# Performance work log

Hardware: AMD Instinct MI355X
Metric: run time of the kernel (lower is better)

The kernel has to match this reference:

```python
import jax, jax.numpy as jnp
import numpy as np

N, E, F, DE, G, C = 50000, 800000, 64, 32, 512, 2
EPS = 1e-5


def setup_inputs() -> dict:
    key = jax.random.key(0)
    ks = jax.random.split(key, 12)
    Z = 2 * F + DE  # CGConv concat dim [x_i, x_j, edge_attr]
    inp = {
        "x": jax.random.normal(ks[0], (N, F), dtype=jnp.float32),
        "edge_index": jax.random.randint(ks[1], (2, E), 0, N, dtype=jnp.int32),
        "edge_attr": jax.random.normal(ks[2], (E, DE), dtype=jnp.float32),
        "batch": jnp.sort(jax.random.randint(ks[3], (N,), 0, G, dtype=jnp.int32)),
        # CGConv lin_f / lin_s : (2F+De) -> F, with bias
        "Wf": jax.random.normal(ks[4], (Z, F), dtype=jnp.float32) * 0.05,
        "bf": jnp.zeros((F,), dtype=jnp.float32),
        "Ws": jax.random.normal(ks[5], (Z, F), dtype=jnp.float32) * 0.05,
        "bs": jnp.zeros((F,), dtype=jnp.float32),
        # CGConv internal BatchNorm (training-mode batch stats)
        "bn_w": jnp.ones((F,), dtype=jnp.float32),
        "bn_b": jnp.zeros((F,), dtype=jnp.float32),
        # PyG LayerNorm (graph mode, batch=None -> whole-tensor stats)
        "ln_w": jnp.ones((F,), dtype=jnp.float32),
        "ln_b": jnp.zeros((F,), dtype=jnp.float32),
        # final linear (2F -> C) and output LayerNorm
        "Wl": jax.random.normal(ks[6], (2 * F, C), dtype=jnp.float32) * 0.05,
        "bl": jnp.zeros((C,), dtype=jnp.float32),
        "ln4_w": jnp.ones((C,), dtype=jnp.float32),
        "ln4_b": jnp.zeros((C,), dtype=jnp.float32),
    }
    return inp


def _pyg_layernorm(x, w, b):
    # torch_geometric.nn.LayerNorm, mode='graph', batch=None: whole-tensor stats
    xc = x - jnp.mean(x)
    out = xc / (jnp.sqrt(jnp.mean(xc * xc)) + EPS)
    return out * w + b


def reference(x, edge_index, edge_attr, batch, Wf, bf, Ws, bs, bn_w, bn_b,
              ln_w, ln_b, Wl, bl, ln4_w, ln4_b):
    src = edge_index[0]  # x_j (source)
    dst = edge_index[1]  # x_i (target / aggregation index)

    # CGConv message: sigmoid(lin_f(z)) * softplus(lin_s(z)), z=[x_i,x_j,e]
    z = jnp.concatenate([x[dst], x[src], edge_attr], axis=1)  # [E, 2F+De]
    msg = jax.nn.sigmoid(z @ Wf + bf) * jax.nn.softplus(z @ Ws + bs)  # [E,F]

    # scatter-add aggregation to target nodes
    agg = jax.ops.segment_sum(msg, dst, num_segments=N)  # [N,F]

    # CGConv batch_norm=True (training-mode batch statistics over nodes)
    mu = jnp.mean(agg, axis=0)
    var = jnp.mean((agg - mu) ** 2, axis=0)
    agg = (agg - mu) / jnp.sqrt(var + EPS) * bn_w + bn_b

    # residual
    h = agg + x

    # LayerNorm + softplus
    h = jax.nn.softplus(_pyg_layernorm(h, ln_w, ln_b))

    # global mean / add pooling over graphs
    add_pool = jax.ops.segment_sum(h, batch, num_segments=G)  # [G,F]
    counts = jax.ops.segment_sum(jnp.ones((N,), h.dtype), batch, num_segments=G)
    mean_pool = add_pool / jnp.maximum(counts, 1.0)[:, None]

    g = jnp.concatenate([mean_pool, add_pool], axis=1)  # [G, 2F]
    out = g @ Wl + bl  # [G, C]
    out = _pyg_layernorm(out, ln4_w, ln4_b)
    return out
```

## Files before the change

kernel.cpp:

```cpp
#include <hip/hip_runtime.h>
#include <math.h>

#define EPSF 1e-5f

typedef short bf16x8 __attribute__((ext_vector_type(8)));
typedef float f32x4 __attribute__((ext_vector_type(4)));

static __device__ __forceinline__ unsigned short f2bf(float x) {
  unsigned u = __float_as_uint(x);
  unsigned r = (u + 0x7FFFu + ((u >> 16) & 1u)) >> 16;
  return (unsigned short)r;
}

static __device__ __forceinline__ float msgv(float F, float S) {
  float sig = __builtin_amdgcn_rcpf(1.0f + __expf(-F));
  float sp = fmaxf(S, 0.f) + __logf(1.0f + __expf(-fabsf(S)));
  return sig * sp;
}

static __device__ __forceinline__ void gload16(const void* g, void* l) {
  __builtin_amdgcn_global_load_lds(
      (const __attribute__((address_space(1))) unsigned int*)g,
      (__attribute__((address_space(3))) unsigned int*)l, 16, 0, 0);
}

__global__ __launch_bounds__(256) void prep_kernel(
    const float* __restrict__ x, const float* __restrict__ Wf,
    const float* __restrict__ Ws, const int* __restrict__ ei,
    unsigned short* __restrict__ xbf, unsigned short* __restrict__ Bfrag,
    int* __restrict__ deg, int NCV, int total8, int E) {
  const int b = blockIdx.x, t = threadIdx.x;
  if (b < NCV) {
    int i = b * 256 + t;
    if (i < total8) {
      float4 a = ((const float4*)x)[i * 2];
      float4 c = ((const float4*)x)[i * 2 + 1];
      unsigned short o[8];
      o[0] = f2bf(a.x); o[1] = f2bf(a.y); o[2] = f2bf(a.z); o[3] = f2bf(a.w);
      o[4] = f2bf(c.x); o[5] = f2bf(c.y); o[6] = f2bf(c.z); o[7] = f2bf(c.w);
      ((uint4*)xbf)[i] = *(uint4*)o;
    }
  } else if (b < NCV + 10) {
    int g2 = (b - NCV) * 256 + t;
    if (g2 < 2560) {
      const int ks = g2 >> 9, t8 = (g2 >> 6) & 7, l = g2 & 63;
      const int q = l & 15, g = l >> 4;
      const float* W = (t8 < 4) ? Wf : Ws;
      const int col = (t8 & 3) * 16 + q;
      unsigned short out[8];
#pragma unroll
      for (int i = 0; i < 8; ++i) {
        int kk = ks * 32 + g * 8 + i;
        int wr = (kk < 32) ? (128 + kk) : (kk - 32);
        out[i] = f2bf(W[(size_t)wr * 64 + col]);
      }
      *(uint4*)&Bfrag[((size_t)(ks * 8 + t8) * 64 + l) * 8] = *(uint4*)out;
    }
  } else {
    int i = (b - NCV - 10) * 256 + t;
    if (i < E) atomicAdd(&deg[ei[E + i]], 1);
  }
}

__global__ __launch_bounds__(256) void scan_a(const int* __restrict__ deg,
                                              int* __restrict__ bsum, int N) {
  const int idx = blockIdx.x * 256 + threadIdx.x;
  int v = (idx < N) ? ((deg[idx] + 15) >> 4) : 0;
#pragma unroll
  for (int o = 32; o > 0; o >>= 1) v += __shfl_down(v, o);
  __shared__ int ws4[4];
  if ((threadIdx.x & 63) == 0) ws4[threadIdx.x >> 6] = v;
  __syncthreads();
  if (threadIdx.x == 0) bsum[blockIdx.x] = ws4[0] + ws4[1] + ws4[2] + ws4[3];
}

__global__ __launch_bounds__(256) void scan_b(const int* __restrict__ bsum,
                                              int* __restrict__ bpre,
                                              int* __restrict__ tile_total,
                                              int NB) {
  const int t = threadIdx.x;
  const int lane = t & 63, w = t >> 6;
  int v = (t < NB) ? bsum[t] : 0;
  int sc = v;
#pragma unroll
  for (int o = 1; o < 64; o <<= 1) {
    int u = __shfl_up(sc, o);
    if (lane >= o) sc += u;
  }
  __shared__ int wsum[4];
  if (lane == 63) wsum[w] = sc;
  __syncthreads();
  int add = 0;
#pragma unroll
  for (int k = 0; k < 4; ++k) add += (k < w) ? wsum[k] : 0;
  bpre[t] = (sc - v) + add;
  if (t == 255) tile_total[0] = sc + add;
}

__global__ __launch_bounds__(256) void scan_c(const int* __restrict__ deg,
                                              const int* __restrict__ bpre,
                                              int* __restrict__ cursor,
                                              int* __restrict__ tstart, int N) {
  const int t = threadIdx.x;
  const int lane = t & 63, w = t >> 6;
  const int idx = blockIdx.x * 256 + t;
  int d = (idx < N) ? ((deg[idx] + 15) >> 4) : 0;
  int sc = d;
#pragma unroll
  for (int o = 1; o < 64; o <<= 1) {
    int u = __shfl_up(sc, o);
    if (lane >= o) sc += u;
  }
  __shared__ int wsum[4];
  if (lane == 63) wsum[w] = sc;
  __syncthreads();
  int add = bpre[blockIdx.x];
#pragma unroll
  for (int k = 0; k < 4; ++k) add += (k < w) ? wsum[k] : 0;
  if (idx < N) {
    int ts = add + (sc - d);
    tstart[idx] = ts;
    cursor[idx] = ts * 16;
  }
}

__global__ __launch_bounds__(256) void scatter_pack(
    const int* __restrict__ ei, int* __restrict__ cursor,
    const int* __restrict__ deg, const int* __restrict__ tstart,
    const float* __restrict__ eattr, int* __restrict__ epk,
    int* __restrict__ thdr, unsigned short* __restrict__ eabf, int E) {
  int i = blockIdx.x * 256 + threadIdx.x;
  if (i >= E) return;
  const int src = ei[i];
  const int dst = ei[E + i];
  const int pos = atomicAdd(&cursor[dst], 1);
  epk[pos] = (src & 0xFFFF) | (dst << 16);
  const int ts = tstart[dst];
  const int k = pos - ts * 16;
  if ((k & 15) == 0) {
    int vc = min(16, deg[dst] - (k & ~15));
    thdr[ts + (k >> 4)] = dst | (vc << 16);
  }
  const float4* er = (const float4*)(eattr + (size_t)i * 32);
  unsigned short o[32];
#pragma unroll
  for (int kk = 0; kk < 8; ++kk) {
    float4 v = er[kk];
    o[kk * 4] = f2bf(v.x); o[kk * 4 + 1] = f2bf(v.y);
    o[kk * 4 + 2] = f2bf(v.z); o[kk * 4 + 3] = f2bf(v.w);
  }
  uint4* dp = (uint4*)(eabf + (size_t)pos * 32);
#pragma unroll
  for (int kk = 0; kk < 4; ++kk) dp[kk] = ((uint4*)o)[kk];
}

__global__ __launch_bounds__(256) void edge_fused(
    const int* __restrict__ epk, const int* __restrict__ thdr,
    const unsigned short* __restrict__ eabf,
    const unsigned short* __restrict__ xbf,
    const unsigned short* __restrict__ Bfrag, const float* __restrict__ bf_,
    const float* __restrict__ bs_, float* __restrict__ agg,
    const int* __restrict__ tile_total, int N) {
  __shared__ __align__(16) unsigned char Bls[40960];
  __shared__ __align__(16) unsigned char AshA[40960];

  for (int i = threadIdx.x; i < 2560; i += 256)
    ((uint4*)Bls)[i] = ((const uint4*)Bfrag)[i];
  __syncthreads();

  const int lane = threadIdx.x & 63, w = threadIdx.x >> 6;
  const int q = lane & 15, g = lane >> 4;
  const int row = lane >> 2, c = lane & 3;
  const int cs = c ^ ((row >> 1) & 3);

  const int T = tile_total[0];
  const int nB = gridDim.x;
  const int cb = (blockIdx.x & 7) * (nB >> 3) + (blockIdx.x >> 3);
  const int qT = T / nB, rT = T - qT * nB;
  const int bt0 = cb * qT + min(cb, rT);
  const int bt1 = bt0 + qT + (cb < rT ? 1 : 0);
  const int blen = bt1 - bt0;
  const int per = (blen + 3) >> 2;
  const int wt0 = bt0 + w * per;
  const int wt1 = min(bt1, wt0 + per);
  if (wt0 >= wt1) return;
  const int tlast = wt1 - 1;

  float bfv[4], bsv[4];
#pragma unroll
  for (int cg = 0; cg < 4; ++cg) {
    bfv[cg] = bf_[cg * 16 + q];
    bsv[cg] = bs_[cg * 16 + q];
  }

  char* myA = (char*)AshA + w * 10240;

  auto STAGE = [&](int bufSel, int tile, int er) {
    unsigned su = (unsigned)(er & 0xFFFF);
    if (su >= (unsigned)N) su = 0;
    unsigned du = ((unsigned)er) >> 16;
    if (du >= (unsigned)N) du = 0;
    char* base = myA + bufSel * 5120;
    gload16(eabf + ((size_t)tile * 16 + row) * 32 + cs * 8, base);
    gload16(xbf + (size_t)du * 64 + cs * 8, base + 1024);
    gload16(xbf + (size_t)du * 64 + 32 + cs * 8, base + 2048);
    gload16(xbf + (size_t)su * 64 + cs * 8, base + 3072);
    gload16(xbf + (size_t)su * 64 + 32 + cs * 8, base + 4096);
  };

  atomicAdd(&agg[lane], 0.0f);
  int tcur = wt0;
  int ep_c = epk[(size_t)tcur * 16 + row];
  int hdr_cur = thdr[tcur];
  STAGE(0, tcur, ep_c);
  const int t1i = min(tcur + 1, tlast);
  int ep_next = epk[(size_t)t1i * 16 + row];
  int hdr_next = thdr[t1i];
  int buf = 0;

  for (;;) {
    const int tn = min(tcur + 1, tlast);
    const int t2i = min(tcur + 2, tlast);
    STAGE(buf ^ 1, tn, ep_next);
    int ep_nn = epk[(size_t)t2i * 16 + row];
    int hdr_nn = thdr[t2i];
    __builtin_amdgcn_sched_barrier(0);
    asm volatile("s_waitcnt vmcnt(8)" ::: "memory");
    __builtin_amdgcn_sched_barrier(0);

    const char* Ab = myA + buf * 5120;
    f32x4 accf[4], accs[4];
#pragma unroll
    for (int nt = 0; nt < 4; ++nt) {
      accf[nt] = (f32x4){0.f, 0.f, 0.f, 0.f};
      accs[nt] = (f32x4){0.f, 0.f, 0.f, 0.f};
    }
#pragma unroll
    for (int ks = 0; ks < 5; ++ks) {
      const bf16x8 a =
          *(const bf16x8*)(Ab + ks * 1024 + q * 64 + ((g ^ ((q >> 1) & 3)) << 4));
#pragma unroll
      for (int nt = 0; nt < 4; ++nt) {
        const bf16x8 Bfr =
            *(const bf16x8*)(Bls + (((ks * 8 + nt) * 64 + lane) << 4));
        const bf16x8 Bsr =
            *(const bf16x8*)(Bls + (((ks * 8 + 4 + nt) * 64 + lane) << 4));
        accf[nt] =
            __builtin_amdgcn_mfma_f32_16x16x32_bf16(a, Bfr, accf[nt], 0, 0, 0);
        accs[nt] =
            __builtin_amdgcn_mfma_f32_16x16x32_bf16(a, Bsr, accs[nt], 0, 0, 0);
      }
    }

    const int dstT = hdr_cur & 0xFFFF;
    const int vcnt = hdr_cur >> 16;
    float tot0, tot1, tot2, tot3;
#pragma unroll
    for (int cg = 0; cg < 4; ++cg) {
      float s = 0.f;
#pragma unroll
      for (int r = 0; r < 4; ++r) {
        float m = msgv(accf[cg][r] + bfv[cg], accs[cg][r] + bsv[cg]);
        s += (g * 4 + r < vcnt) ? m : 0.f;
      }
      s += __shfl_xor(s, 16);
      s += __shfl_xor(s, 32);
      if (cg == 0) tot0 = s;
      else if (cg == 1) tot1 = s;
      else if (cg == 2) tot2 = s;
      else tot3 = s;
    }
    float v = (g == 0) ? tot0 : (g == 1) ? tot1 : (g == 2) ? tot2 : tot3;
    unsigned dd = (unsigned)dstT;
    float vv = (dd < (unsigned)N) ? v : 0.f;
    dd = min(dd, (unsigned)(N - 1));
    atomicAdd(&agg[(size_t)dd * 64 + g * 16 + q], vv);

    if (tcur == tlast) break;
    tcur += 1;
    buf ^= 1;
    hdr_cur = hdr_next;
    hdr_next = hdr_nn;
    ep_next = ep_nn;
  }
}

__global__ __launch_bounds__(256) void stats_kernel(
    const float* __restrict__ agg, const float* __restrict__ x,
    float* __restrict__ stats, int N) {
  const int f = threadIdx.x & 63;
  const int sub = threadIdx.x >> 6;
  float sa = 0, sa2 = 0, sx = 0, sx2 = 0, sax = 0;
  for (int r = blockIdx.x * 4 + sub; r < N; r += gridDim.x * 4) {
    float a = agg[(size_t)r * 64 + f];
    float xv = x[(size_t)r * 64 + f];
    sa += a; sa2 += a * a; sx += xv; sx2 += xv * xv; sax += a * xv;
  }
  __shared__ float lds[4][5][64];
  lds[sub][0][f] = sa; lds[sub][1][f] = sa2; lds[sub][2][f] = sx;
  lds[sub][3][f] = sx2; lds[sub][4][f] = sax;
  __syncthreads();
  if (sub == 0) {
#pragma unroll
    for (int i = 0; i < 5; ++i) {
      float v = lds[0][i][f] + lds[1][i][f] + lds[2][i][f] + lds[3][i][f];
      atomicAdd(&stats[i * 64 + f], v);
    }
  }
}

__global__ __launch_bounds__(256) void node_finish(
    const float* __restrict__ stats, const float* __restrict__ bn_w,
    const float* __restrict__ bn_b, const float* __restrict__ agg,
    const float* __restrict__ x, const int* __restrict__ batch,
    const float* __restrict__ ln_w, const float* __restrict__ ln_b,
    float* __restrict__ add_pool, float* __restrict__ counts, int N,
    int chunk) {
  const int f = threadIdx.x & 63;
  const int sub = threadIdx.x >> 6;
  const float Nf = (float)N;
  const float invN = 1.0f / Nf;
  float Sa = stats[f], Sa2 = stats[64 + f], Sx = stats[128 + f],
        Sx2 = stats[192 + f], Sax = stats[256 + f];
  float mu = Sa * invN;
  float var = Sa2 * invN - mu * mu;
  const float alpha = bn_w[f] / sqrtf(var + EPSF);
  const float beta = bn_b[f] - mu * alpha;
  float Sh = alpha * Sa + Nf * beta + Sx;
  float Sh2 = alpha * alpha * Sa2 + Sx2 + Nf * beta * beta +
              2.f * alpha * Sax + 2.f * alpha * beta * Sa + 2.f * beta * Sx;
#pragma unroll
  for (int o = 32; o > 0; o >>= 1) {
    Sh += __shfl_xor(Sh, o);
    Sh2 += __shfl_xor(Sh2, o);
  }
  const float cnt = Nf * 64.0f;
  const float mean = Sh / cnt;
  const float msq = Sh2 / cnt - mean * mean;
  const float rden = 1.0f / (sqrtf(fmaxf(msq, 0.f)) + EPSF);
  const float lw = ln_w[f] * rden;
  const float lb = ln_b[f];

  const int r0 = blockIdx.x * chunk;
  const int r1 = min(N, r0 + chunk);
  float acc = 0.f, cacc = 0.f;
  int curg = -1;
  for (int r = r0 + sub; r < r1; r += 4) {
    int g = batch[r];
    if (g != curg) {
      if (curg >= 0) {
        atomicAdd(&add_pool[(size_t)curg * 64 + f], acc);
        if (f == 0) atomicAdd(&counts[curg], cacc);
      }
      curg = g; acc = 0.f; cacc = 0.f;
    }
    float h = fmaf(alpha, agg[(size_t)r * 64 + f], beta) + x[(size_t)r * 64 + f];
    float v = (h - mean) * lw + lb;
    float sp = fmaxf(v, 0.f) + __logf(1.0f + __expf(-fabsf(v)));
    acc += sp; cacc += 1.f;
  }
  if (curg >= 0) {
    atomicAdd(&add_pool[(size_t)curg * 64 + f], acc);
    if (f == 0) atomicAdd(&counts[curg], cacc);
  }
}

__global__ __launch_bounds__(1024) void graph_out(
    const float* __restrict__ add_pool, const float* __restrict__ counts,
    const float* __restrict__ Wl, const float* __restrict__ bl,
    const float* __restrict__ w4, const float* __restrict__ b4,
    float* __restrict__ out, int G) {
  const int t = threadIdx.x;
  const int g = t >> 1, c = t & 1;
  float cnt = fmaxf(counts[g], 1.0f);
  float inv = 1.0f / cnt;
  const float4* ap4 = (const float4*)(add_pool + (size_t)g * 64);
  const float4* W4 = (const float4*)Wl;
  float v = bl[c];
#pragma unroll 4
  for (int k4 = 0; k4 < 16; ++k4) {
    float4 a4 = ap4[k4];
    float4 wa = W4[k4 * 2];
    float4 wb = W4[k4 * 2 + 1];
    float4 wc = W4[32 + k4 * 2];
    float4 wd = W4[32 + k4 * 2 + 1];
    float m0 = c ? wa.y : wa.x, m1 = c ? wa.w : wa.z;
    float m2 = c ? wb.y : wb.x, m3 = c ? wb.w : wb.z;
    float a0 = c ? wc.y : wc.x, a1 = c ? wc.w : wc.z;
    float a2 = c ? wd.y : wd.x, a3 = c ? wd.w : wd.z;
    v = fmaf(a4.x, fmaf(m0, inv, a0), v);
    v = fmaf(a4.y, fmaf(m1, inv, a1), v);
    v = fmaf(a4.z, fmaf(m2, inv, a2), v);
    v = fmaf(a4.w, fmaf(m3, inv, a3), v);
  }

  __shared__ float red[16];
  __shared__ float bc[2];
  float sum = v;
#pragma unroll
  for (int o = 32; o > 0; o >>= 1) sum += __shfl_down(sum, o);
  if ((t & 63) == 0) red[t >> 6] = sum;
  __syncthreads();
  if (t == 0) {
    float tot = 0;
#pragma unroll
    for (int i = 0; i < 16; ++i) tot += red[i];
    bc[0] = tot * (1.0f / 1024.0f);
  }
  __syncthreads();
  const float mean = bc[0];
  const float xc = v - mean;
  float sq = xc * xc;
  __syncthreads();
#pragma unroll
  for (int o = 32; o > 0; o >>= 1) sq += __shfl_down(sq, o);
  if ((t & 63) == 0) red[t >> 6] = sq;
  __syncthreads();
  if (t == 0) {
    float tot = 0;
#pragma unroll
    for (int i = 0; i < 16; ++i) tot += red[i];
    bc[1] = 1.0f / (sqrtf(tot * (1.0f / 1024.0f)) + EPSF);
  }
  __syncthreads();
  out[t] = xc * bc[1] * w4[c] + b4[c];
}

extern "C" void kernel_launch(void* const* d_in, const int* in_sizes, int n_in,
                              void* d_out, int out_size, void* d_ws,
                              size_t ws_size, hipStream_t stream) {
  const float* x = (const float*)d_in[0];
  const int* ei = (const int*)d_in[1];
  const float* eattr = (const float*)d_in[2];
  const int* batch = (const int*)d_in[3];
  const float* Wf = (const float*)d_in[4];
  const float* bf = (const float*)d_in[5];
  const float* Ws = (const float*)d_in[6];
  const float* bs = (const float*)d_in[7];
  const float* bn_w = (const float*)d_in[8];
  const float* bn_b = (const float*)d_in[9];
  const float* ln_w = (const float*)d_in[10];
  const float* ln_b = (const float*)d_in[11];
  const float* Wl = (const float*)d_in[12];
  const float* bl = (const float*)d_in[13];
  const float* w4 = (const float*)d_in[14];
  const float* b4 = (const float*)d_in[15];

  const int N = in_sizes[0] / 64;
  const int E = in_sizes[2] / 32;
  const int G = 512;
  const int NB = (N + 255) / 256;
  const int NCV = (N * 8 + 255) / 256;
  const int NH = (E + 255) / 256;
  const int Tcap = N + (E + 15) / 16;

  float* ws = (float*)d_ws;
  float* agg = ws;
  float* stats = agg + (size_t)N * 64;
  float* add_pool = stats + 320;
  float* counts = add_pool + (size_t)G * 64;
  int* deg = (int*)(counts + G);
  int* cursor = deg + N;
  int* tstart = cursor + N;
  int* tile_total = tstart + N;
  int* bsum = tile_total + 4;
  int* bpre = bsum + 256;
  unsigned short* Bfrag = (unsigned short*)(bpre + 256);
  unsigned short* xbf = Bfrag + 20480;
  int* thdr = (int*)(xbf + (size_t)N * 64);
  int* epk = thdr + Tcap;
  unsigned short* eabf = (unsigned short*)(epk + (size_t)Tcap * 16);

  size_t zeroFloats = (size_t)N * 64 + 320 + (size_t)G * 64 + G + N;
  hipMemsetAsync(agg, 0, zeroFloats * sizeof(float), stream);
  hipMemsetAsync(epk, 0, (size_t)Tcap * 16 * sizeof(int), stream);

  prep_kernel<<<NCV + 10 + NH, 256, 0, stream>>>(x, Wf, Ws, ei, xbf, Bfrag,
                                                 deg, NCV, N * 8, E);
  scan_a<<<NB, 256, 0, stream>>>(deg, bsum, N);
  scan_b<<<1, 256, 0, stream>>>(bsum, bpre, tile_total, NB);
  scan_c<<<NB, 256, 0, stream>>>(deg, bpre, cursor, tstart, N);
  scatter_pack<<<NH, 256, 0, stream>>>(ei, cursor, deg, tstart, eattr, epk,
                                       thdr, eabf, E);
  edge_fused<<<512, 256, 0, stream>>>(epk, thdr, eabf, xbf, Bfrag, bf, bs, agg,
                                      tile_total, N);
  stats_kernel<<<512, 256, 0, stream>>>(agg, x, stats, N);
  const int chunk = (N + 511) / 512;
  node_finish<<<512, 256, 0, stream>>>(stats, bn_w, bn_b, agg, x, batch, ln_w,
                                       ln_b, add_pool, counts, N, chunk);
  graph_out<<<1, 1024, 0, stream>>>(add_pool, counts, Wl, bl, w4, b4,
                                    (float*)d_out, G);
}
```

Measured before the change: 323.1 us.

## Precompute per-node destination projection and drop x_i from the edge GEMM

Every edge in a tile shares the same destination node, so the x_i part of lin_f and lin_s (plus bias) is computed once per node by a new node_mfma kernel into a float2 buffer. The edge kernel then runs a 96-wide K GEMM (edge_attr plus x_j) instead of 160, stages less data into LDS, and adds the per-node projection loaded from global memory. LDS use per block drops, so the edge grid is raised from 512 to 768 blocks. The cost is an extra kernel launch and a 25.6MB float2 buffer, now written once and read per tile, and the vmcnt wait is retuned to match the new load count.

```diff
diff --git a/kernel.cpp b/kernel.cpp
--- a/kernel.cpp
+++ b/kernel.cpp
@@ -28,7 +28,8 @@
     const float* __restrict__ x, const float* __restrict__ Wf,
     const float* __restrict__ Ws, const int* __restrict__ ei,
     unsigned short* __restrict__ xbf, unsigned short* __restrict__ Bfrag,
-    int* __restrict__ deg, int NCV, int total8, int E) {
+    unsigned short* __restrict__ Bfrag2, int* __restrict__ deg, int NCV,
+    int total8, int E) {
   const int b = blockIdx.x, t = threadIdx.x;
   if (b < NCV) {
     int i = b * 256 + t;
@@ -40,9 +41,9 @@
       o[4] = f2bf(c.x); o[5] = f2bf(c.y); o[6] = f2bf(c.z); o[7] = f2bf(c.w);
       ((uint4*)xbf)[i] = *(uint4*)o;
     }
-  } else if (b < NCV + 10) {
+  } else if (b < NCV + 6) {
     int g2 = (b - NCV) * 256 + t;
-    if (g2 < 2560) {
+    if (g2 < 1536) {
       const int ks = g2 >> 9, t8 = (g2 >> 6) & 7, l = g2 & 63;
       const int q = l & 15, g = l >> 4;
       const float* W = (t8 < 4) ? Wf : Ws;
@@ -51,14 +52,71 @@
 #pragma unroll
       for (int i = 0; i < 8; ++i) {
         int kk = ks * 32 + g * 8 + i;
-        int wr = (kk < 32) ? (128 + kk) : (kk - 32);
+        int wr = (kk < 32) ? (128 + kk) : (32 + kk);
         out[i] = f2bf(W[(size_t)wr * 64 + col]);
       }
       *(uint4*)&Bfrag[((size_t)(ks * 8 + t8) * 64 + l) * 8] = *(uint4*)out;
     }
+  } else if (b < NCV + 10) {
+    int g2 = (b - NCV - 6) * 256 + t;
+    if (g2 < 1024) {
+      const int ks = g2 >> 9, t8 = (g2 >> 6) & 7, l = g2 & 63;
+      const int q = l & 15, g = l >> 4;
+      const float* W = (t8 < 4) ? Wf : Ws;
+      const int col = (t8 & 3) * 16 + q;
+      unsigned short out[8];
+#pragma unroll
+      for (int i = 0; i < 8; ++i) {
+        int kk = ks * 32 + g * 8 + i;
+        out[i] = f2bf(W[(size_t)kk * 64 + col]);
+      }
+      *(uint4*)&Bfrag2[((size_t)(ks * 8 + t8) * 64 + l) * 8] = *(uint4*)out;
+    }
   } else {
     int i = (b - NCV - 10) * 256 + t;
     if (i < E) atomicAdd(&deg[ei[E + i]], 1);
+  }
+}
+
+__global__ __launch_bounds__(256, 4) void node_mfma(
+    const unsigned short* __restrict__ xbf,
+    const unsigned short* __restrict__ Bfrag2, const float* __restrict__ bf_,
+    const float* __restrict__ bs_, float2* __restrict__ Pd2, int N) {
+  __shared__ __align__(16) short Bsh[16][64][8];
+  for (int i = threadIdx.x; i < 1024; i += 256)
+    ((uint4*)Bsh)[i] = ((const uint4*)Bfrag2)[i];
+  __syncthreads();
+  const int lane = threadIdx.x & 63, w = threadIdx.x >> 6;
+  const int q = lane & 15, g = lane >> 4;
+  const int row0 = blockIdx.x * 64;
+  const float bfv = bf_[w * 16 + q], bsv = bs_[w * 16 + q];
+  f32x4 accf[4], accs[4];
+#pragma unroll
+  for (int mt = 0; mt < 4; ++mt) {
+    accf[mt] = (f32x4){0.f, 0.f, 0.f, 0.f};
+    accs[mt] = (f32x4){0.f, 0.f, 0.f, 0.f};
+  }
+#pragma unroll
+  for (int ks = 0; ks < 2; ++ks) {
+    const bf16x8 Bfr = *(const bf16x8*)&Bsh[ks * 8 + w][lane][0];
+    const bf16x8 Bsr = *(const bf16x8*)&Bsh[ks * 8 + 4 + w][lane][0];
+#pragma unroll
+    for (int mt = 0; mt < 4; ++mt) {
+      int row = min(row0 + mt * 16 + q, N - 1);
+      const bf16x8 a = *(const bf16x8*)(xbf + (size_t)row * 64 + ks * 32 + g * 8);
+      accf[mt] = __builtin_amdgcn_mfma_f32_16x16x32_bf16(a, Bfr, accf[mt], 0, 0, 0);
+      accs[mt] = __builtin_amdgcn_mfma_f32_16x16x32_bf16(a, Bsr, accs[mt], 0, 0, 0);
+    }
+  }
+#pragma unroll
+  for (int mt = 0; mt < 4; ++mt) {
+#pragma unroll
+    for (int r = 0; r < 4; ++r) {
+      int row = row0 + mt * 16 + g * 4 + r;
+      if (row < N)
+        Pd2[(size_t)row * 64 + w * 16 + q] =
+            make_float2(accf[mt][r] + bfv, accs[mt][r] + bsv);
+    }
   }
 }
 
@@ -158,13 +216,12 @@
     const int* __restrict__ epk, const int* __restrict__ thdr,
     const unsigned short* __restrict__ eabf,
     const unsigned short* __restrict__ xbf,
-    const unsigned short* __restrict__ Bfrag, const float* __restrict__ bf_,
-    const float* __restrict__ bs_, float* __restrict__ agg,
-    const int* __restrict__ tile_total, int N) {
-  __shared__ __align__(16) unsigned char Bls[40960];
-  __shared__ __align__(16) unsigned char AshA[40960];
-
-  for (int i = threadIdx.x; i < 2560; i += 256)
+    const unsigned short* __restrict__ Bfrag, const float2* __restrict__ Pd2,
+    float* __restrict__ agg, const int* __restrict__ tile_total, int N) {
+  __shared__ __align__(16) unsigned char Bls[24576];
+  __shared__ __align__(16) unsigned char AshA[24576];
+
+  for (int i = threadIdx.x; i < 1536; i += 256)
     ((uint4*)Bls)[i] = ((const uint4*)Bfrag)[i];
   __syncthreads();
 
@@ -186,49 +243,43 @@
   if (wt0 >= wt1) return;
   const int tlast = wt1 - 1;
 
-  float bfv[4], bsv[4];
-#pragma unroll
-  for (int cg = 0; cg < 4; ++cg) {
-    bfv[cg] = bf_[cg * 16 + q];
-    bsv[cg] = bs_[cg * 16 + q];
-  }
-
-  char* myA = (char*)AshA + w * 10240;
-
-  auto STAGE = [&](int bufSel, int tile, int er) {
+  char* myA = (char*)AshA + w * 6144;
+
+  auto STAGE = [&](int bufSel, int tile, int er, int hdr, float2 (&pd)[4]) {
     unsigned su = (unsigned)(er & 0xFFFF);
     if (su >= (unsigned)N) su = 0;
-    unsigned du = ((unsigned)er) >> 16;
+    unsigned du = (unsigned)(hdr & 0xFFFF);
     if (du >= (unsigned)N) du = 0;
-    char* base = myA + bufSel * 5120;
+    char* base = myA + bufSel * 3072;
     gload16(eabf + ((size_t)tile * 16 + row) * 32 + cs * 8, base);
-    gload16(xbf + (size_t)du * 64 + cs * 8, base + 1024);
-    gload16(xbf + (size_t)du * 64 + 32 + cs * 8, base + 2048);
-    gload16(xbf + (size_t)su * 64 + cs * 8, base + 3072);
-    gload16(xbf + (size_t)su * 64 + 32 + cs * 8, base + 4096);
+    gload16(xbf + (size_t)su * 64 + cs * 8, base + 1024);
+    gload16(xbf + (size_t)su * 64 + 32 + cs * 8, base + 2048);
+#pragma unroll
+    for (int nt = 0; nt < 4; ++nt) pd[nt] = Pd2[(size_t)du * 64 + nt * 16 + q];
   };
 
   atomicAdd(&agg[lane], 0.0f);
   int tcur = wt0;
+  int hdr_cur = thdr[tcur];
   int ep_c = epk[(size_t)tcur * 16 + row];
-  int hdr_cur = thdr[tcur];
-  STAGE(0, tcur, ep_c);
+  float2 pd_cur[4], pd_nxt[4];
+  STAGE(0, tcur, ep_c, hdr_cur, pd_cur);
   const int t1i = min(tcur + 1, tlast);
-  int ep_next = epk[(size_t)t1i * 16 + row];
-  int hdr_next = thdr[t1i];
+  int ep_n = epk[(size_t)t1i * 16 + row];
+  int hdr_n = thdr[t1i];
   int buf = 0;
 
   for (;;) {
     const int tn = min(tcur + 1, tlast);
     const int t2i = min(tcur + 2, tlast);
-    STAGE(buf ^ 1, tn, ep_next);
+    STAGE(buf ^ 1, tn, ep_n, hdr_n, pd_nxt);
     int ep_nn = epk[(size_t)t2i * 16 + row];
     int hdr_nn = thdr[t2i];
     __builtin_amdgcn_sched_barrier(0);
-    asm volatile("s_waitcnt vmcnt(8)" ::: "memory");
+    asm volatile("s_waitcnt vmcnt(15)" ::: "memory");
     __builtin_amdgcn_sched_barrier(0);
 
-    const char* Ab = myA + buf * 5120;
+    const char* Ab = myA + buf * 3072;
     f32x4 accf[4], accs[4];
 #pragma unroll
     for (int nt = 0; nt < 4; ++nt) {
@@ -236,7 +287,7 @@
       accs[nt] = (f32x4){0.f, 0.f, 0.f, 0.f};
     }
 #pragma unroll
-    for (int ks = 0; ks < 5; ++ks) {
+    for (int ks = 0; ks < 3; ++ks) {
       const bf16x8 a =
           *(const bf16x8*)(Ab + ks * 1024 + q * 64 + ((g ^ ((q >> 1) & 3)) << 4));
 #pragma unroll
@@ -260,7 +311,7 @@
       float s = 0.f;
 #pragma unroll
       for (int r = 0; r < 4; ++r) {
-        float m = msgv(accf[cg][r] + bfv[cg], accs[cg][r] + bsv[cg]);
+        float m = msgv(accf[cg][r] + pd_cur[cg].x, accs[cg][r] + pd_cur[cg].y);
         s += (g * 4 + r < vcnt) ? m : 0.f;
       }
       s += __shfl_xor(s, 16);
@@ -279,9 +330,11 @@
     if (tcur == tlast) break;
     tcur += 1;
     buf ^= 1;
-    hdr_cur = hdr_next;
-    hdr_next = hdr_nn;
-    ep_next = ep_nn;
+    hdr_cur = hdr_n;
+    hdr_n = hdr_nn;
+    ep_n = ep_nn;
+#pragma unroll
+    for (int nt = 0; nt < 4; ++nt) pd_cur[nt] = pd_nxt[nt];
   }
 }
 
@@ -466,8 +519,10 @@
   int* bsum = tile_total + 4;
   int* bpre = bsum + 256;
   unsigned short* Bfrag = (unsigned short*)(bpre + 256);
-  unsigned short* xbf = Bfrag + 20480;
-  int* thdr = (int*)(xbf + (size_t)N * 64);
+  unsigned short* Bfrag2 = Bfrag + 12288;
+  unsigned short* xbf = Bfrag2 + 8192;
+  float2* Pd2 = (float2*)(xbf + (size_t)N * 64);
+  int* thdr = (int*)(Pd2 + (size_t)N * 64);
   int* epk = thdr + Tcap;
   unsigned short* eabf = (unsigned short*)(epk + (size_t)Tcap * 16);
 
@@ -476,13 +531,14 @@
   hipMemsetAsync(epk, 0, (size_t)Tcap * 16 * sizeof(int), stream);
 
   prep_kernel<<<NCV + 10 + NH, 256, 0, stream>>>(x, Wf, Ws, ei, xbf, Bfrag,
-                                                 deg, NCV, N * 8, E);
+                                                 Bfrag2, deg, NCV, N * 8, E);
+  node_mfma<<<(N + 63) / 64, 256, 0, stream>>>(xbf, Bfrag2, bf, bs, Pd2, N);
   scan_a<<<NB, 256, 0, stream>>>(deg, bsum, N);
   scan_b<<<1, 256, 0, stream>>>(bsum, bpre, tile_total, NB);
   scan_c<<<NB, 256, 0, stream>>>(deg, bpre, cursor, tstart, N);
   scatter_pack<<<NH, 256, 0, stream>>>(ei, cursor, deg, tstart, eattr, epk,
                                        thdr, eabf, E);
-  edge_fused<<<512, 256, 0, stream>>>(epk, thdr, eabf, xbf, Bfrag, bf, bs, agg,
+  edge_fused<<<768, 256, 0, stream>>>(epk, thdr, eabf, xbf, Bfrag, Pd2, agg,
                                       tile_total, N);
   stats_kernel<<<512, 256, 0, stream>>>(agg, x, stats, N);
   const int chunk = (N + 511) / 512;
```

Result: slower. 369.9 us (+14.5%).
